# Kernel optimization log

Hardware: AMD Instinct MI355X
Metric: run time of the kernel (lower is better)

Reference implementation:

```python
import jax, jax.numpy as jnp
import numpy as np

W = 256            # square image side (in_size)
N_ANGLES = 180     # theta = arange(180) degrees (default)
STEPS = 5


def _make_grids():
    # torch.affine_grid with R=[[cos,sin,0],[-sin,cos,0]], align_corners=False
    th = np.deg2rad(np.arange(N_ANGLES, dtype=np.float32))
    coords = (2.0 * np.arange(W, dtype=np.float32) + 1.0) / W - 1.0  # pixel centers in [-1,1]
    xg, yg = np.meshgrid(coords, coords)          # xg varies along cols, yg along rows
    cos = np.cos(th)[:, None, None]
    sin = np.sin(th)[:, None, None]
    gx = cos * xg + sin * yg
    gy = -sin * xg + cos * yg
    return jnp.asarray(np.stack([gx, gy], axis=-1))  # [A,W,W,2]

GRIDS = _make_grids()


def _grid_sample(img, grid):
    # img [N,W,W], grid [A,W,W,2]; bilinear, zeros padding, align_corners=False
    gx, gy = grid[..., 0], grid[..., 1]
    ix = ((gx + 1.0) * W - 1.0) * 0.5
    iy = ((gy + 1.0) * W - 1.0) * 0.5
    ix0 = jnp.floor(ix)
    iy0 = jnp.floor(iy)
    wx1 = ix - ix0
    wy1 = iy - iy0

    def gather(iyf, ixf):
        valid = (ixf >= 0) & (ixf < W) & (iyf >= 0) & (iyf < W)
        ixc = jnp.clip(ixf, 0, W - 1).astype(jnp.int32)
        iyc = jnp.clip(iyf, 0, W - 1).astype(jnp.int32)
        v = img[:, iyc, ixc]                     # [N,A,W,W]
        return jnp.where(valid, v, jnp.float32(0.0))

    return ((1.0 - wy1) * ((1.0 - wx1) * gather(iy0, ix0) + wx1 * gather(iy0, ix0 + 1))
            + wy1 * ((1.0 - wx1) * gather(iy0 + 1, ix0) + wx1 * gather(iy0 + 1, ix0 + 1)))


def _forward(x, index):
    img = x[:, 0]                                # [N,W,W] (C==1)
    rot = _grid_sample(img, GRIDS)               # [N,A,W(rows),W(cols)]
    segments = np.linspace(1, W / 2, STEPS + 1).astype(int)  # matches torch linspace dtype=int
    ran = np.abs(np.arange(W) - (W - 1) / 2.0)
    outs = []
    for step in range(2):
        t = segments[4 - index + step]
        m = (ran < t).astype(np.float32)
        m = jnp.asarray(m / m.sum())             # normalized hard mask over rows
        outs.append(jnp.einsum('narc,r->nca', rot, m))  # [N,W,A]
    return jnp.stack(outs, axis=1)               # [N,2,W,A]


def setup_inputs() -> dict:
    key = jax.random.key(0)
    x = jax.random.normal(key, (4, 1, W, W), dtype=jnp.float32)
    return {"x": x, "index": 2}


def reference(x, index):
    return _forward(x, index)
```

## Files before the change

kernel.cpp:

```cpp
#include <hip/hip_runtime.h>
#include <hip/hip_fp16.h>

#define W 256
#define NA 180
#define SPLIT 4
#define ROWBYTES 580
#define ROWS 259

__global__ __launch_bounds__(1024, 4) void radon_kernel(
    const float* __restrict__ x, const int* __restrict__ index_p,
    float* __restrict__ out)
{
    __shared__ __half simg[ROWS * 290];

    const int a = blockIdx.x;
    const int n = blockIdx.y;
    const int tid = threadIdx.x;
    const int c = tid & (W - 1);
    const int s = tid >> 8;

    const float* __restrict__ img = x + (size_t)n * W * W;

    {
        unsigned* wp = (unsigned*)simg;
        if (tid < 435) {
            const int rr = tid / 145;
            const int w = tid - rr * 145;
            const int row = (rr == 0) ? 0 : (256 + rr);
            wp[row * 145 + w] = 0u;
        } else if (tid < 947) {
            const int i = tid - 435;
            const int row = 1 + (i >> 1);
            const int w = (i & 1) ? 129 : 0;
            wp[row * 145 + w] = 0u;
        }
    }

    {
        const float4* img4 = (const float4*)img;
        #pragma unroll
        for (int k = 0; k < 16; ++k) {
            const int g = k * 1024 + tid;
            const int row = (g >> 6) + 1;
            const int m = g & 63;
            const float4 v = img4[g];
            const __half2 h01 = __floats2half2_rn(v.x, v.y);
            const __half2 h23 = __floats2half2_rn(v.z, v.w);
            char* base = (char*)simg + row * ROWBYTES + 8 * m + 4;
            *(unsigned*)(base)     = *(const unsigned*)&h01;
            *(unsigned*)(base + 4) = *(const unsigned*)&h23;
        }
    }
    __syncthreads();

    const int index = *index_p;
    const int seg[6] = {1, 26, 51, 77, 102, 128};
    const int t0 = seg[4 - index];
    const int t1 = seg[4 - index + 1];

    float sa, ca;
    sincosf((float)a * 0.017453292519943295f, &sa, &ca);

    const float xc = ((2.0f * (float)c + 1.0f) * (1.0f / (float)W)) - 1.0f;
    const float bx = fmaf(128.0f * ca, xc, 127.5f + 2.0f);
    const float by = fmaf(-128.0f * sa, xc, 127.5f + 1.0f);

    const int r1lo = 128 - t1;
    const int r0lo = 128 - t0, r0hi = 127 + t0;
    const int total = 2 * t1;
    const int chunk = (total + SPLIT - 1) / SPLIT;
    const int rs = r1lo + s * chunk;
    const int re = min(rs + chunk, r1lo + total);

    const char* S = (const char*)simg;

#define TAP_BODY                                                              \
        float ix = fmaf(sa, rf, bx);                                          \
        float iy = fmaf(ca, rf, by);                                          \
        ix = __builtin_amdgcn_fmed3f(ix, 1.0f, 258.0f);                       \
        iy = __builtin_amdgcn_fmed3f(iy, 0.0f, 257.0f);                       \
        const float wx = __builtin_amdgcn_fractf(ix);  \
        const float wy = __builtin_amdgcn_fractf(iy);                         \
        const int x0 = (int)ix;                  \
        const int y0 = (int)iy;                                               \
        const int sh = (x0 & 1) << 4;                                         \
        const char* p = S + (y0 * ROWBYTES + (x0 >> 1) * 4);                  \
        const unsigned A0 = *(const unsigned*)(p);                            \
        const unsigned A1 = *(const unsigned*)(p + ROWBYTES);                 \
        const unsigned B0 = *(const unsigned*)(p + 4);                        \
        const unsigned B1 = *(const unsigned*)(p + ROWBYTES + 4);             \
        const unsigned q0 = (unsigned)(((((unsigned long long)B0) << 32) | A0) >> sh); \
        const unsigned q1 = (unsigned)(((((unsigned long long)B1) << 32) | A1) >> sh); \
        const __half2 h0 = *(const __half2*)&q0;                              \
        const __half2 h1 = *(const __half2*)&q1;                              \
        const float v00 = __low2float(h0);                                    \
        const float v01 = __high2float(h0);                                   \
        const float v10 = __low2float(h1);                                    \
        const float v11 = __high2float(h1);                                   \
        const float top = fmaf(wx, v01 - v00, v00);                           \
        const float bot = fmaf(wx, v11 - v10, v10);                           \
        const float val = fmaf(wy, bot - top, top);

    float sumA = 0.0f, sumB = 0.0f, sumC = 0.0f;

    {
        const int e = min(re, r0lo);
        float rf = (float)rs - 127.5f;
        #pragma unroll 8
        for (int r = rs; r < e; ++r, rf += 1.0f) { TAP_BODY sumA += val; }
    }
    {
        const int b = max(rs, r0lo);
        const int e = min(re, r0hi + 1);
        float rf = (float)b - 127.5f;
        #pragma unroll 8
        for (int r = b; r < e; ++r, rf += 1.0f) { TAP_BODY sumB += val; }
    }
    {
        const int b = max(rs, r0hi + 1);
        float rf = (float)b - 127.5f;
        #pragma unroll 8
        for (int r = b; r < re; ++r, rf += 1.0f) { TAP_BODY sumC += val; }
    }
#undef TAP_BODY

    const float sum0 = sumB;
    const float sum1 = sumA + sumB + sumC;

    __syncthreads();
    float* red = (float*)simg;
    red[(0 * SPLIT + s) * W + c] = sum0;
    red[(1 * SPLIT + s) * W + c] = sum1;
    __syncthreads();

    if (s == 0) {
        const float acc0 = red[0 * W + c] + red[1 * W + c] + red[2 * W + c] + red[3 * W + c];
        const float* r1p = red + SPLIT * W;
        const float acc1 = r1p[0 * W + c] + r1p[1 * W + c] + r1p[2 * W + c] + r1p[3 * W + c];
        out[(((size_t)n * 2 + 0) * W + c) * NA + a] = acc0 * (1.0f / (float)(2 * t0));
        out[(((size_t)n * 2 + 1) * W + c) * NA + a] = acc1 * (1.0f / (float)(2 * t1));
    }
}

extern "C" void kernel_launch(void* const* d_in, const int* in_sizes, int n_in,
                              void* d_out, int out_size, void* d_ws, size_t ws_size,
                              hipStream_t stream) {
    const float* x = (const float*)d_in[0];
    const int* index_p = (const int*)d_in[1];
    float* out = (float*)d_out;
    const int N = in_sizes[0] / (W * W);
    dim3 grid(NA, N);
    radon_kernel<<<grid, 1024, 0, stream>>>(x, index_p, out);
}
```

Before: 46.53 us.

## Split image rows across two blocks per angle with half-size LDS and atomic accumulation

Each (angle, image) pair is now handled by two blocks, each staging only half of the image rows in LDS. A per-column split point along the ray is computed so each block samples only taps whose source row lies in its half, and partial sums are combined with atomicAdd into an output zeroed by a memset. Halving LDS per block is meant to allow more resident blocks and better latency hiding, and each block loads only half the image from global memory. In exchange it adds a memset launch, atomic traffic, split-point search loops, and load imbalance between threads within a block.

```diff
diff --git a/kernel.cpp b/kernel.cpp
--- a/kernel.cpp
+++ b/kernel.cpp
@@ -5,16 +5,18 @@
 #define NA 180
 #define SPLIT 4
 #define ROWBYTES 580
-#define ROWS 259
+#define HROWS 130
 
-__global__ __launch_bounds__(1024, 4) void radon_kernel(
+
+__global__ __launch_bounds__(1024, 8) void radon_kernel(
     const float* __restrict__ x, const int* __restrict__ index_p,
     float* __restrict__ out)
 {
-    __shared__ __half simg[ROWS * 290];
+    __shared__ __half simg[HROWS * 290];
 
     const int a = blockIdx.x;
     const int n = blockIdx.y;
+    const int h = blockIdx.z;
     const int tid = threadIdx.x;
     const int c = tid & (W - 1);
     const int s = tid >> 8;
@@ -23,30 +25,37 @@
 
     {
         unsigned* wp = (unsigned*)simg;
-        if (tid < 435) {
-            const int rr = tid / 145;
-            const int w = tid - rr * 145;
-            const int row = (rr == 0) ? 0 : (256 + rr);
+        if (tid < 260) {
+            const int row = tid >> 1;
+            const int w = (tid & 1) ? 129 : 0;
             wp[row * 145 + w] = 0u;
-        } else if (tid < 947) {
-            const int i = tid - 435;
-            const int row = 1 + (i >> 1);
-            const int w = (i & 1) ? 129 : 0;
-            wp[row * 145 + w] = 0u;
+        } else {
+            const int i = tid - 260;
+            if (h == 0) {
+                if (i < 145) wp[i] = 0u;
+            } else {
+                if (i < 290) {
+                    const int row = 128 + (i >= 145);
+                    const int w = (i >= 145) ? (i - 145) : i;
+                    wp[row * 145 + w] = 0u;
+                }
+            }
         }
     }
 
     {
-        const float4* img4 = (const float4*)img;
-        #pragma unroll
-        for (int k = 0; k < 16; ++k) {
-            const int g = k * 1024 + tid;
-            const int row = (g >> 6) + 1;
+        const int ps = h ? 128 : 0;
+        const int nrows = h ? 128 : 129;
+        const int lbias = h ? -128 : 1;
+        const float4* img4 = (const float4*)(img + ps * W);
+        const int ngroups = nrows * 64;
+        for (int g = tid; g < ngroups; g += 1024) {
+            const int rr = g >> 6;
             const int m = g & 63;
             const float4 v = img4[g];
             const __half2 h01 = __floats2half2_rn(v.x, v.y);
             const __half2 h23 = __floats2half2_rn(v.z, v.w);
-            char* base = (char*)simg + row * ROWBYTES + 8 * m + 4;
+            char* base = (char*)simg + (rr + ps + lbias) * ROWBYTES + 8 * m + 4;
             *(unsigned*)(base)     = *(const unsigned*)&h01;
             *(unsigned*)(base + 4) = *(const unsigned*)&h23;
         }
@@ -62,26 +71,56 @@
     sincosf((float)a * 0.017453292519943295f, &sa, &ca);
 
     const float xc = ((2.0f * (float)c + 1.0f) * (1.0f / (float)W)) - 1.0f;
-    const float bx = fmaf(128.0f * ca, xc, 127.5f + 2.0f);
-    const float by = fmaf(-128.0f * sa, xc, 127.5f + 1.0f);
+    const float bx  = fmaf(128.0f * ca, xc, 127.5f + 2.0f);
+    const float byg = fmaf(-128.0f * sa, xc, 127.5f + 1.0f);
+    const float byh = byg - 129.0f * (float)h;
+    const float yup = h ? 128.0f : 257.0f;
 
-    const int r1lo = 128 - t1;
+    const int r1lo = 128 - t1, r1hi = 127 + t1;
     const int r0lo = 128 - t0, r0hi = 127 + t0;
-    const int total = 2 * t1;
-    const int chunk = (total + SPLIT - 1) / SPLIT;
-    const int rs = r1lo + s * chunk;
-    const int re = min(rs + chunk, r1lo + total);
+
+    int lo, hi;
+    {
+        float t = 127.5f + (129.0f - byg) / ca;
+        t = __builtin_amdgcn_fmed3f(t, (float)(r1lo - 1), (float)(r1hi + 1));
+        int rsp = (int)t;
+#define PRED(r) (__builtin_amdgcn_fmed3f(fmaf(ca, (float)(r) - 127.5f, byg), 0.0f, 257.0f) < 129.0f)
+        if (ca >= 0.0f) {
+            rsp = min(max(rsp, r1lo - 1), r1hi);
+            while (rsp < r1hi && PRED(rsp + 1)) ++rsp;
+            while (rsp >= r1lo && !PRED(rsp)) --rsp;
+            lo = h ? rsp + 1 : r1lo;
+            hi = h ? r1hi : rsp;
+        } else {
+            rsp = min(max(rsp, r1lo), r1hi + 1);
+            while (rsp > r1lo && PRED(rsp - 1)) --rsp;
+            while (rsp <= r1hi && !PRED(rsp)) ++rsp;
+            lo = h ? r1lo : rsp;
+            hi = h ? rsp - 1 : r1hi;
+        }
+#undef PRED
+    }
+
+    int rs, re;
+    {
+        const int len = hi - lo + 1;
+        if (len > 0) {
+            const int chunk = (len + SPLIT - 1) / SPLIT;
+            rs = lo + s * chunk;
+            re = min(rs + chunk, lo + len);
+        } else { rs = 0; re = 0; }
+    }
 
     const char* S = (const char*)simg;
 
 #define TAP_BODY                                                              \
         float ix = fmaf(sa, rf, bx);                                          \
-        float iy = fmaf(ca, rf, by);                                          \
+        float iy = fmaf(ca, rf, byh);                                         \
         ix = __builtin_amdgcn_fmed3f(ix, 1.0f, 258.0f);                       \
-        iy = __builtin_amdgcn_fmed3f(iy, 0.0f, 257.0f);                       \
-        const float wx = __builtin_amdgcn_fractf(ix);  \
+        iy = __builtin_amdgcn_fmed3f(iy, 0.0f, yup);                          \
+        const float wx = __builtin_amdgcn_fractf(ix);                         \
         const float wy = __builtin_amdgcn_fractf(iy);                         \
-        const int x0 = (int)ix;                  \
+        const int x0 = (int)ix;                                               \
         const int y0 = (int)iy;                                               \
         const int sh = (x0 & 1) << 4;                                         \
         const char* p = S + (y0 * ROWBYTES + (x0 >> 1) * 4);                  \
@@ -91,35 +130,34 @@
         const unsigned B1 = *(const unsigned*)(p + ROWBYTES + 4);             \
         const unsigned q0 = (unsigned)(((((unsigned long long)B0) << 32) | A0) >> sh); \
         const unsigned q1 = (unsigned)(((((unsigned long long)B1) << 32) | A1) >> sh); \
-        const __half2 h0 = *(const __half2*)&q0;                              \
-        const __half2 h1 = *(const __half2*)&q1;                              \
-        const float v00 = __low2float(h0);                                    \
-        const float v01 = __high2float(h0);                                   \
-        const float v10 = __low2float(h1);                                    \
-        const float v11 = __high2float(h1);                                   \
+        const __half2 h0v = *(const __half2*)&q0;                             \
+        const __half2 h1v = *(const __half2*)&q1;                             \
+        const float v00 = __low2float(h0v);                                   \
+        const float v01 = __high2float(h0v);                                  \
+        const float v10 = __low2float(h1v);                                   \
+        const float v11 = __high2float(h1v);                                  \
         const float top = fmaf(wx, v01 - v00, v00);                           \
         const float bot = fmaf(wx, v11 - v10, v10);                           \
         const float val = fmaf(wy, bot - top, top);
 
     float sumA = 0.0f, sumB = 0.0f, sumC = 0.0f;
-
     {
         const int e = min(re, r0lo);
         float rf = (float)rs - 127.5f;
-        #pragma unroll 8
+        #pragma unroll 4
         for (int r = rs; r < e; ++r, rf += 1.0f) { TAP_BODY sumA += val; }
     }
     {
         const int b = max(rs, r0lo);
         const int e = min(re, r0hi + 1);
         float rf = (float)b - 127.5f;
-        #pragma unroll 8
+        #pragma unroll 4
         for (int r = b; r < e; ++r, rf += 1.0f) { TAP_BODY sumB += val; }
     }
     {
         const int b = max(rs, r0hi + 1);
         float rf = (float)b - 127.5f;
-        #pragma unroll 8
+        #pragma unroll 4
         for (int r = b; r < re; ++r, rf += 1.0f) { TAP_BODY sumC += val; }
     }
 #undef TAP_BODY
@@ -137,8 +175,8 @@
         const float acc0 = red[0 * W + c] + red[1 * W + c] + red[2 * W + c] + red[3 * W + c];
         const float* r1p = red + SPLIT * W;
         const float acc1 = r1p[0 * W + c] + r1p[1 * W + c] + r1p[2 * W + c] + r1p[3 * W + c];
-        out[(((size_t)n * 2 + 0) * W + c) * NA + a] = acc0 * (1.0f / (float)(2 * t0));
-        out[(((size_t)n * 2 + 1) * W + c) * NA + a] = acc1 * (1.0f / (float)(2 * t1));
+        atomicAdd(out + (((size_t)n * 2 + 0) * W + c) * NA + a, acc0 * (1.0f / (float)(2 * t0)));
+        atomicAdd(out + (((size_t)n * 2 + 1) * W + c) * NA + a, acc1 * (1.0f / (float)(2 * t1)));
     }
 }
 
@@ -149,6 +187,9 @@
     const int* index_p = (const int*)d_in[1];
     float* out = (float*)d_out;
     const int N = in_sizes[0] / (W * W);
-    dim3 grid(NA, N);
+
+    hipMemsetAsync(d_out, 0, (size_t)out_size * sizeof(float), stream);
+
+    dim3 grid(NA, N, 2);
     radon_kernel<<<grid, 1024, 0, stream>>>(x, index_p, out);
 }
```

After: 66.40 us. +42.7%, slower.

## Split image into row halves per block with ray clipping and atomic accumulation

Applied to the files above, without the earlier changes.

Each block now stages only half of the image (128 rows plus padding) in shared memory, and the grid gains a third dimension for the two halves. Each wavefront computes the range of ray steps whose samples fall inside its half and splits only that range across the four thread groups. Partial sums are combined with atomicAdd into an output that is zeroed first with hipMemsetAsync. The goal is to halve LDS use per block so more blocks fit per CU, and to skip taps outside the slab. The cost is twice as many blocks, duplicated sincos setup, atomic traffic, an extra memset launch, and a window computation that divides by cos(angle), which can be near zero.

```diff
diff --git a/kernel.cpp b/kernel.cpp
--- a/kernel.cpp
+++ b/kernel.cpp
@@ -4,51 +4,48 @@
 #define W 256
 #define NA 180
 #define SPLIT 4
-#define ROWBYTES 580
-#define ROWS 259
+#define RWORDS 145
+#define LROWS 131
+#define SWORDS (LROWS * RWORDS)
 
-__global__ __launch_bounds__(1024, 4) void radon_kernel(
+
+__global__ __launch_bounds__(1024, 8) void radon_kernel(
     const float* __restrict__ x, const int* __restrict__ index_p,
     float* __restrict__ out)
 {
-    __shared__ __half simg[ROWS * 290];
+    __shared__ unsigned sw[SWORDS];
 
     const int a = blockIdx.x;
     const int n = blockIdx.y;
+    const int h = blockIdx.z;
     const int tid = threadIdx.x;
     const int c = tid & (W - 1);
     const int s = tid >> 8;
 
-    const float* __restrict__ img = x + (size_t)n * W * W;
-
-    {
-        unsigned* wp = (unsigned*)simg;
-        if (tid < 435) {
-            const int rr = tid / 145;
-            const int w = tid - rr * 145;
-            const int row = (rr == 0) ? 0 : (256 + rr);
-            wp[row * 145 + w] = 0u;
-        } else if (tid < 947) {
-            const int i = tid - 435;
-            const int row = 1 + (i >> 1);
-            const int w = (i & 1) ? 129 : 0;
-            wp[row * 145 + w] = 0u;
-        }
+    if (tid < 435) {
+        const int rr = tid / 145;
+        const int w = tid - rr * 145;
+        const int row = (rr == 0) ? 0 : (128 + rr);
+        sw[row * RWORDS + w] = 0u;
+    } else if (tid < 691) {
+        const int i = tid - 435;
+        const int row = 1 + (i >> 1);
+        const int w = (i & 1) ? 129 : 0;
+        sw[row * RWORDS + w] = 0u;
     }
 
     {
-        const float4* img4 = (const float4*)img;
+        const float4* img4 = (const float4*)(x + (size_t)n * W * W + h * 128 * W);
         #pragma unroll
-        for (int k = 0; k < 16; ++k) {
+        for (int k = 0; k < 8; ++k) {
             const int g = k * 1024 + tid;
-            const int row = (g >> 6) + 1;
+            const int lr = (g >> 6) + 1;
             const int m = g & 63;
             const float4 v = img4[g];
             const __half2 h01 = __floats2half2_rn(v.x, v.y);
             const __half2 h23 = __floats2half2_rn(v.z, v.w);
-            char* base = (char*)simg + row * ROWBYTES + 8 * m + 4;
-            *(unsigned*)(base)     = *(const unsigned*)&h01;
-            *(unsigned*)(base + 4) = *(const unsigned*)&h23;
+            sw[lr * RWORDS + 2 * m + 1] = *(const unsigned*)&h01;
+            sw[lr * RWORDS + 2 * m + 2] = *(const unsigned*)&h23;
         }
     }
     __syncthreads();
@@ -62,64 +59,80 @@
     sincosf((float)a * 0.017453292519943295f, &sa, &ca);
 
     const float xc = ((2.0f * (float)c + 1.0f) * (1.0f / (float)W)) - 1.0f;
-    const float bx = fmaf(128.0f * ca, xc, 127.5f + 2.0f);
-    const float by = fmaf(-128.0f * sa, xc, 127.5f + 1.0f);
+    const float bx  = fmaf(128.0f * ca, xc, 129.5f);
+    const float byg = fmaf(-128.0f * sa, xc, 128.5f);
+    const float byh = byg - 128.0f * (float)h;
 
-    const int r1lo = 128 - t1;
+    const int r1lo = 128 - t1, r1hi = 127 + t1;
     const int r0lo = 128 - t0, r0hi = 127 + t0;
-    const int total = 2 * t1;
-    const int chunk = (total + SPLIT - 1) / SPLIT;
-    const int rs = r1lo + s * chunk;
-    const int re = min(rs + chunk, r1lo + total);
 
-    const char* S = (const char*)simg;
+    int rs = 0, re = 0;
+    {
+        const float inv = 1.0f / ca;
+        const float b0 = fmaf(-1.0f - byh, inv, 127.5f);
+        const float b1 = fmaf(130.0f - byh, inv, 127.5f);
+        float lo_f = fminf(b0, b1), hi_f = fmaxf(b0, b1);
+        lo_f = __builtin_amdgcn_fmed3f(lo_f, -1.0f, 400.0f);
+        hi_f = __builtin_amdgcn_fmed3f(hi_f, -1.0f, 400.0f);
+        int wl = max((int)floorf(lo_f), r1lo);
+        int wh = min((int)ceilf(hi_f), r1hi);
+        const int l0 = __shfl(wl, 0), l63 = __shfl(wl, 63);
+        const int u0 = __shfl(wh, 0), u63 = __shfl(wh, 63);
+        wl = min(l0, l63);
+        wh = max(u0, u63);
+        const int len = wh - wl + 1;
+        if (len > 0) {
+            const int chunk = (len + SPLIT - 1) / SPLIT;
+            rs = wl + s * chunk;
+            re = min(rs + chunk, wl + len);
+        }
+    }
 
 #define TAP_BODY                                                              \
-        float ix = fmaf(sa, rf, bx);                                          \
-        float iy = fmaf(ca, rf, by);                                          \
-        ix = __builtin_amdgcn_fmed3f(ix, 1.0f, 258.0f);                       \
-        iy = __builtin_amdgcn_fmed3f(iy, 0.0f, 257.0f);                       \
-        const float wx = __builtin_amdgcn_fractf(ix);  \
-        const float wy = __builtin_amdgcn_fractf(iy);                         \
-        const int x0 = (int)ix;                  \
-        const int y0 = (int)iy;                                               \
+        float ixf = fmaf(sa, rf, bx);                                         \
+        float iyf = fmaf(ca, rf, byh);                                        \
+        ixf = __builtin_amdgcn_fmed3f(ixf, 1.0f, 258.0f);                     \
+        iyf = __builtin_amdgcn_fmed3f(iyf, 0.0f, 129.0f);                     \
+        const float wx = __builtin_amdgcn_fractf(ixf);                        \
+        const float wy = __builtin_amdgcn_fractf(iyf);                        \
+        const int x0 = (int)ixf;                                              \
+        const int y0 = (int)iyf;                                              \
+        const int wi = y0 * RWORDS + (x0 >> 1);                               \
+        const unsigned A0 = sw[wi];                                           \
+        const unsigned B0 = sw[wi + 1];                                       \
+        const unsigned A1 = sw[wi + RWORDS];                                  \
+        const unsigned B1 = sw[wi + RWORDS + 1];                              \
         const int sh = (x0 & 1) << 4;                                         \
-        const char* p = S + (y0 * ROWBYTES + (x0 >> 1) * 4);                  \
-        const unsigned A0 = *(const unsigned*)(p);                            \
-        const unsigned A1 = *(const unsigned*)(p + ROWBYTES);                 \
-        const unsigned B0 = *(const unsigned*)(p + 4);                        \
-        const unsigned B1 = *(const unsigned*)(p + ROWBYTES + 4);             \
         const unsigned q0 = (unsigned)(((((unsigned long long)B0) << 32) | A0) >> sh); \
         const unsigned q1 = (unsigned)(((((unsigned long long)B1) << 32) | A1) >> sh); \
-        const __half2 h0 = *(const __half2*)&q0;                              \
-        const __half2 h1 = *(const __half2*)&q1;                              \
-        const float v00 = __low2float(h0);                                    \
-        const float v01 = __high2float(h0);                                   \
-        const float v10 = __low2float(h1);                                    \
-        const float v11 = __high2float(h1);                                   \
+        const __half2 h0v = *(const __half2*)&q0;                             \
+        const __half2 h1v = *(const __half2*)&q1;                             \
+        const float v00 = __low2float(h0v);                                   \
+        const float v01 = __high2float(h0v);                                  \
+        const float v10 = __low2float(h1v);                                   \
+        const float v11 = __high2float(h1v);                                  \
         const float top = fmaf(wx, v01 - v00, v00);                           \
         const float bot = fmaf(wx, v11 - v10, v10);                           \
         const float val = fmaf(wy, bot - top, top);
 
     float sumA = 0.0f, sumB = 0.0f, sumC = 0.0f;
-
     {
         const int e = min(re, r0lo);
         float rf = (float)rs - 127.5f;
-        #pragma unroll 8
+        #pragma unroll 4
         for (int r = rs; r < e; ++r, rf += 1.0f) { TAP_BODY sumA += val; }
     }
     {
         const int b = max(rs, r0lo);
         const int e = min(re, r0hi + 1);
         float rf = (float)b - 127.5f;
-        #pragma unroll 8
+        #pragma unroll 4
         for (int r = b; r < e; ++r, rf += 1.0f) { TAP_BODY sumB += val; }
     }
     {
         const int b = max(rs, r0hi + 1);
         float rf = (float)b - 127.5f;
-        #pragma unroll 8
+        #pragma unroll 4
         for (int r = b; r < re; ++r, rf += 1.0f) { TAP_BODY sumC += val; }
     }
 #undef TAP_BODY
@@ -128,7 +141,7 @@
     const float sum1 = sumA + sumB + sumC;
 
     __syncthreads();
-    float* red = (float*)simg;
+    float* red = (float*)sw;
     red[(0 * SPLIT + s) * W + c] = sum0;
     red[(1 * SPLIT + s) * W + c] = sum1;
     __syncthreads();
@@ -137,8 +150,8 @@
         const float acc0 = red[0 * W + c] + red[1 * W + c] + red[2 * W + c] + red[3 * W + c];
         const float* r1p = red + SPLIT * W;
         const float acc1 = r1p[0 * W + c] + r1p[1 * W + c] + r1p[2 * W + c] + r1p[3 * W + c];
-        out[(((size_t)n * 2 + 0) * W + c) * NA + a] = acc0 * (1.0f / (float)(2 * t0));
-        out[(((size_t)n * 2 + 1) * W + c) * NA + a] = acc1 * (1.0f / (float)(2 * t1));
+        atomicAdd(out + (((size_t)n * 2 + 0) * W + c) * NA + a, acc0 * (1.0f / (float)(2 * t0)));
+        atomicAdd(out + (((size_t)n * 2 + 1) * W + c) * NA + a, acc1 * (1.0f / (float)(2 * t1)));
     }
 }
 
@@ -149,6 +162,9 @@
     const int* index_p = (const int*)d_in[1];
     float* out = (float*)d_out;
     const int N = in_sizes[0] / (W * W);
-    dim3 grid(NA, N);
+
+    hipMemsetAsync(d_out, 0, (size_t)out_size * sizeof(float), stream);
+
+    dim3 grid(NA, N, 2);
     radon_kernel<<<grid, 1024, 0, stream>>>(x, index_p, out);
 }
```

New measurement: 61.24 us. 1.32x slower.
